# Kernel optimization log

Measured on AMD Instinct MI355X. Metric: run time of the kernel, lower is better.

## Reference

```python
import jax, jax.numpy as jnp
import numpy as np

EMBED = 768
HEADS = 12
HEAD_DIM = EMBED // HEADS
NUM_BUCKETS = 32
MAX_DISTANCE = 128


def _relative_buckets(tgt_len, src_len):
    ctx = jnp.arange(tgt_len)[:, None]
    mem = jnp.arange(src_len)[None, :]
    rel = mem - ctx                                  # [T, S]
    nb = NUM_BUCKETS // 2                            # 16
    buckets = (rel > 0).astype(jnp.int32) * nb
    rp = jnp.abs(rel)
    max_exact = nb // 2                              # 8
    is_small = rp < max_exact
    rp_safe = jnp.maximum(rp, 1).astype(jnp.float32)
    large = max_exact + (
        jnp.log(rp_safe / max_exact) / np.log(MAX_DISTANCE / max_exact) * (nb - max_exact)
    ).astype(jnp.int32)
    large = jnp.minimum(large, nb - 1)
    buckets = buckets + jnp.where(is_small, rp, large)
    return buckets                                   # [T, S] int32


def setup_inputs() -> dict:
    key = jax.random.key(0)
    ks = jax.random.split(key, 12)
    T, B, E = 2048, 2, EMBED
    def xavier(k, shape, gain=1.0):
        fan_in, fan_out = shape[0], shape[1]
        a = gain * np.sqrt(6.0 / (fan_in + fan_out))
        return jax.random.uniform(k, shape, jnp.float32, -a, a)
    g = 1.0 / np.sqrt(2.0)
    return {
        "query": jax.random.normal(ks[0], (T, B, E), jnp.float32),
        "key": jax.random.normal(ks[1], (T, B, E), jnp.float32),
        "value": jax.random.normal(ks[2], (T, B, E), jnp.float32),
        "key_padding_mask": jnp.zeros((B, T), dtype=bool),
        # weights stored [in, out] (transpose of torch Linear)
        "Wq": xavier(ks[3], (E, E), g), "bq": jnp.zeros((E,), jnp.float32),
        "Wk": xavier(ks[4], (E, E), g), "bk": jnp.zeros((E,), jnp.float32),
        "Wv": xavier(ks[5], (E, E), g), "bv": jnp.zeros((E,), jnp.float32),
        "Wo": xavier(ks[6], (E, E), 1.0), "bo": jnp.zeros((E,), jnp.float32),
        "rel_bias": jax.random.normal(ks[7], (NUM_BUCKETS, HEADS), jnp.float32)
        * np.sqrt(2.0 / (NUM_BUCKETS + HEADS)),
    }


def reference(query, key, value, key_padding_mask, Wq, bq, Wk, bk, Wv, bv, Wo, bo, rel_bias):
    T, B, E = query.shape
    S = key.shape[0]
    scaling = HEAD_DIM ** -0.5
    q = (query @ Wq + bq) * scaling
    k = key @ Wk + bk
    v = value @ Wv + bv
    # [T,B,E] -> [B,H,T,D]
    def split_heads(x, L):
        return x.reshape(L, B, HEADS, HEAD_DIM).transpose(1, 2, 0, 3)
    qh, kh, vh = split_heads(q, T), split_heads(k, S), split_heads(v, S)
    # T5 relative position bias: [H, T, S]
    buckets = _relative_buckets(T, S)
    position_bias = rel_bias[buckets].transpose(2, 0, 1)  # [H,T,S]
    scores = jnp.einsum("bhtd,bhsd->bhts", qh, kh) + position_bias[None]
    scores = jnp.where(key_padding_mask[:, None, None, :], -jnp.inf, scores)
    probs = jax.nn.softmax(scores, axis=-1)
    attn = jnp.einsum("bhts,bhsd->bhtd", probs, vh)
    attn = attn.transpose(2, 0, 1, 3).reshape(T, B, E)
    return attn @ Wo + bo
```

## Files before the change

### kernel.cpp

```cpp
#include <hip/hip_runtime.h>
#include <hip/hip_bf16.h>

typedef __bf16 bf16;
typedef __bf16 bf16x8 __attribute__((ext_vector_type(8)));
typedef float f32x4 __attribute__((ext_vector_type(4)));

#define EMB 768
#define NH 12
#define HD 64
#define SEQ 2048
#define NBATCH 2
#define NREL (2 * SEQ - 1)

__device__ __forceinline__ int swz(int bo) { return bo ^ ((bo >> 3) & 0x70); }
__device__ __forceinline__ int swz256(int bo) { return bo ^ ((bo >> 4) & 0x70); }
__device__ __forceinline__ int kpos(int s) {
  return (s & 0x23) | ((s & 0x04) << 2) | ((s & 0x18) >> 1);
}

typedef __attribute__((address_space(3))) unsigned int lds_u32;
typedef __attribute__((address_space(1))) unsigned int glb_u32;
__device__ __forceinline__ void gld16(const void* g, void* l) {
  __builtin_amdgcn_global_load_lds((const glb_u32*)g, (lds_u32*)l, 16, 0, 0);
}

__global__ void k_bias_table(const float* __restrict__ rel_bias,
                             float* __restrict__ bias_tab) {
  int i = blockIdx.x * 256 + threadIdx.x;
  if (i >= NREL) return;
  int rel = i - (SEQ - 1);
  int bkt = (rel > 0) ? 16 : 0;
  int rp = rel < 0 ? -rel : rel;
  if (rp < 8) {
    bkt += rp;
  } else {
    float lf = (logf((float)rp * 0.125f) / 2.7725887222397811f) * 8.0f;
    int large = 8 + (int)lf;
    bkt += (large < 15) ? large : 15;
  }
  for (int h = 0; h < NH; ++h)
    bias_tab[h * NREL + i] = rel_bias[bkt * NH + h];
}

__global__ void k_maskbits(const unsigned char* __restrict__ mask,
                           unsigned long long* __restrict__ mbits) {
  int wid = blockIdx.x * 4 + (threadIdx.x >> 6);
  int lane = threadIdx.x & 63;
  int b = wid >> 5, wd = wid & 31;
  unsigned long long m = __ballot(mask[b * SEQ + wd * 64 + lane] != 0);
  if (lane == 0) mbits[wid] = m;
}

__global__ __launch_bounds__(256) void k_cvt_x(
    const float* __restrict__ Xq, const float* __restrict__ Xk,
    const float* __restrict__ Xv, bf16* __restrict__ ximg) {
  const int z = blockIdx.z;
  const float* X = z == 0 ? Xq : z == 1 ? Xk : Xv;
  const int m0 = blockIdx.x * 128, k0 = blockIdx.y * 64;
  char* img = (char*)ximg + ((size_t)(z * 32 + blockIdx.x) * 12 + blockIdx.y) * 16384;
#pragma unroll
  for (int it = 0; it < 4; ++it) {
    int i = threadIdx.x + it * 256;
    int mr = i >> 3, kc8 = (i & 7) * 8;
    const float* xp = X + (size_t)(m0 + mr) * EMB + k0 + kc8;
    float4 f0 = *(const float4*)xp, f1 = *(const float4*)(xp + 4);
    bf16x8 hh;
    hh[0] = (bf16)f0.x; hh[1] = (bf16)f0.y; hh[2] = (bf16)f0.z; hh[3] = (bf16)f0.w;
    hh[4] = (bf16)f1.x; hh[5] = (bf16)f1.y; hh[6] = (bf16)f1.z; hh[7] = (bf16)f1.w;
    *(bf16x8*)(img + swz(mr * 128 + kc8 * 2)) = hh;
  }
}

__global__ __launch_bounds__(256) void k_cvt_w(
    const float* __restrict__ Wq, const float* __restrict__ Wk,
    const float* __restrict__ Wv, const float* __restrict__ Wo,
    bf16* __restrict__ wimg) {
  __shared__ __align__(16) bf16 T[64 * 128];
  const int z = blockIdx.z;
  const float* W = z == 0 ? Wq : z == 1 ? Wk : z == 2 ? Wv : Wo;
  const int nb = blockIdx.x, ks = blockIdx.y;
  const int n0 = nb * 128, k0 = ks * 64;
  const int tid = threadIdx.x;
  {
    int kk = tid >> 2, nn0 = (tid & 3) * 32;
    const float* wp = W + (size_t)(k0 + kk) * EMB + n0 + nn0;
#pragma unroll
    for (int jq = 0; jq < 4; ++jq) {
      float4 f0 = *(const float4*)(wp + jq * 8);
      float4 f1 = *(const float4*)(wp + jq * 8 + 4);
      bf16x8 hh;
      hh[0] = (bf16)f0.x; hh[1] = (bf16)f0.y; hh[2] = (bf16)f0.z; hh[3] = (bf16)f0.w;
      hh[4] = (bf16)f1.x; hh[5] = (bf16)f1.y; hh[6] = (bf16)f1.z; hh[7] = (bf16)f1.w;
      *(bf16x8*)((char*)T + swz256(kk * 256 + (nn0 + jq * 8) * 2)) = hh;
    }
  }
  __syncthreads();
  {
    int nr = tid >> 1, kh = tid & 1;
    char* img = (char*)wimg + ((size_t)(z * 6 + nb) * 12 + ks) * 16384;
#pragma unroll
    for (int jq = 0; jq < 4; ++jq) {
      union { bf16 e[8]; uint4 u; } pk;
#pragma unroll
      for (int q = 0; q < 8; ++q)
        pk.e[q] = *(const bf16*)((char*)T + swz256((kh * 32 + jq * 8 + q) * 256 + nr * 2));
      *(uint4*)(img + swz(nr * 128 + (kh * 32 + jq * 8) * 2)) = pk.u;
    }
  }
}

__global__ __launch_bounds__(256) void k_proj_qkv(
    const bf16* __restrict__ ximg, const bf16* __restrict__ wimg,
    const float* __restrict__ bq, const float* __restrict__ bk,
    const float* __restrict__ bv, bf16* __restrict__ oq,
    bf16* __restrict__ gk, bf16* __restrict__ gv) {
  __shared__ __align__(16) bf16 AB[2][2][8192];
  const int z = blockIdx.z;
  const float* bias = z == 0 ? bq : z == 1 ? bk : bv;
  const float scale = z == 0 ? 0.125f : 1.0f;
  const int mb = blockIdx.x, nb = blockIdx.y;
  const int m0 = mb * 128, n0 = nb * 128;
  const int tid = threadIdx.x, lane = tid & 63, w = tid >> 6;
  const int c = lane & 15, g = lane >> 4;
  const int mo = (w >> 1) * 64, no = (w & 1) * 64;
  const char* abase = (const char*)ximg + (size_t)(z * 32 + mb) * 12 * 16384;
  const char* bbase = (const char*)wimg + (size_t)(z * 6 + nb) * 12 * 16384;

#define PISSUE(KS, BUF) do {                                               \
    const char* a_ = abase + (size_t)(KS) * 16384;                         \
    const char* b_ = bbase + (size_t)(KS) * 16384;                         \
    _Pragma("unroll") for (int ch = 0; ch < 4; ++ch) {                     \
      int ck = w * 4 + ch;                                                 \
      gld16(a_ + ck * 1024 + lane * 16, (char*)AB[BUF][0] + ck * 1024);    \
      gld16(b_ + ck * 1024 + lane * 16, (char*)AB[BUF][1] + ck * 1024);    \
    }                                                                      \
  } while (0)

  PISSUE(0, 0);
  f32x4 acc[4][4] = {};
  asm volatile("s_waitcnt vmcnt(0)" ::: "memory");
  __syncthreads();
  for (int ks = 0; ks < 12; ++ks) {
    const int cur = ks & 1;
    if (ks < 11) PISSUE(ks + 1, cur ^ 1);
    const char* As = (const char*)AB[cur][0];
    const char* Bs = (const char*)AB[cur][1];
    __builtin_amdgcn_s_setprio(1);
#pragma unroll
    for (int kk = 0; kk < 2; ++kk) {
      bf16x8 av[4], bvf[4];
#pragma unroll
      for (int mf = 0; mf < 4; ++mf)
        av[mf] = *(const bf16x8*)(As + swz((mo + mf * 16 + c) * 128 + kk * 64 + g * 16));
#pragma unroll
      for (int nf = 0; nf < 4; ++nf)
        bvf[nf] = *(const bf16x8*)(Bs + swz((no + nf * 16 + c) * 128 + kk * 64 + g * 16));
#pragma unroll
      for (int mf = 0; mf < 4; ++mf)
#pragma unroll
        for (int nf = 0; nf < 4; ++nf)
          acc[mf][nf] = __builtin_amdgcn_mfma_f32_16x16x32_bf16(bvf[nf], av[mf], acc[mf][nf], 0, 0, 0);
    }
    __builtin_amdgcn_s_setprio(0);
    if (ks < 11) {
      asm volatile("s_waitcnt vmcnt(0)" ::: "memory");
      __syncthreads();
    }
  }
#pragma unroll
  for (int nf = 0; nf < 4; ++nf) {
    int n = n0 + no + nf * 16 + g * 4;
    float4 b4 = *(const float4*)&bias[n];
#pragma unroll
    for (int mf = 0; mf < 4; ++mf) {
      int m = m0 + mo + mf * 16 + c;
      float v0 = (acc[mf][nf][0] + b4.x) * scale;
      float v1 = (acc[mf][nf][1] + b4.y) * scale;
      float v2 = (acc[mf][nf][2] + b4.z) * scale;
      float v3 = (acc[mf][nf][3] + b4.w) * scale;
      if (z == 0) {
        union { bf16 e[4]; uint2 u; } pk;
        pk.e[0] = (bf16)v0; pk.e[1] = (bf16)v1; pk.e[2] = (bf16)v2; pk.e[3] = (bf16)v3;
        *(uint2*)(oq + (size_t)m * EMB + n) = pk.u;
      } else if (z == 1) {
        int t = m >> 1, bb = m & 1;
        int hh = n >> 6, d = n & 63;
        union { bf16 e[4]; uint2 u; } pk;
        pk.e[0] = (bf16)v0; pk.e[1] = (bf16)v1; pk.e[2] = (bf16)v2; pk.e[3] = (bf16)v3;
        char* base = (char*)gk + ((size_t)(bb * NH + hh) * 32 + (t >> 6)) * 8192;
        *(uint2*)(base + swz(kpos(t & 63) * 128 + (d & ~7) * 2) + (d & 4) * 2) = pk.u;
      } else {
        int s = m >> 1, bb = m & 1;
        int hh = n >> 6, d0 = n & 63;
        char* base = (char*)gv + ((size_t)(bb * NH + hh) * 32 + (s >> 6)) * 8192;
        int sc2 = (s & 63) * 2;
        *(bf16*)(base + (((d0 + 0) * 128 + sc2) ^ (((d0 + 0) & 7) << 4))) = (bf16)v0;
        *(bf16*)(base + (((d0 + 1) * 128 + sc2) ^ (((d0 + 1) & 7) << 4))) = (bf16)v1;
        *(bf16*)(base + (((d0 + 2) * 128 + sc2) ^ (((d0 + 2) & 7) << 4))) = (bf16)v2;
        *(bf16*)(base + (((d0 + 3) * 128 + sc2) ^ (((d0 + 3) & 7) << 4))) = (bf16)v3;
      }
    }
  }
#undef PISSUE
}

__global__ __launch_bounds__(256) void k_proj_out(
    const bf16* __restrict__ aimg, const bf16* __restrict__ wimg,
    const float* __restrict__ bias, float* __restrict__ out) {
  __shared__ __align__(16) bf16 AB[2][2][8192];
  const int mb = blockIdx.x, nb = blockIdx.y;
  const int m0 = mb * 128, n0 = nb * 128;
  const int tid = threadIdx.x, lane = tid & 63, w = tid >> 6;
  const int c = lane & 15, g = lane >> 4;
  const int mo = (w >> 1) * 64, no = (w & 1) * 64;
  const char* abase = (const char*)aimg + (size_t)mb * 12 * 16384;
  const char* bbase = (const char*)wimg + (size_t)(3 * 6 + nb) * 12 * 16384;

#define PISSUE(KS, BUF) do {                                               \
    const char* a_ = abase + (size_t)(KS) * 16384;                         \
    const char* b_ = bbase + (size_t)(KS) * 16384;                         \
    _Pragma("unroll") for (int ch = 0; ch < 4; ++ch) {                     \
      int ck = w * 4 + ch;                                                 \
      gld16(a_ + ck * 1024 + lane * 16, (char*)AB[BUF][0] + ck * 1024);    \
      gld16(b_ + ck * 1024 + lane * 16, (char*)AB[BUF][1] + ck * 1024);    \
    }                                                                      \
  } while (0)

  PISSUE(0, 0);
  f32x4 acc[4][4] = {};
  asm volatile("s_waitcnt vmcnt(0)" ::: "memory");
  __syncthreads();
  for (int ks = 0; ks < 12; ++ks) {
    const int cur = ks & 1;
    if (ks < 11) PISSUE(ks + 1, cur ^ 1);
    const char* As = (const char*)AB[cur][0];
    const char* Bs = (const char*)AB[cur][1];
    __builtin_amdgcn_s_setprio(1);
#pragma unroll
    for (int kk = 0; kk < 2; ++kk) {
      bf16x8 av[4], bvf[4];
#pragma unroll
      for (int mf = 0; mf < 4; ++mf)
        av[mf] = *(const bf16x8*)(As + swz((mo + mf * 16 + c) * 128 + kk * 64 + g * 16));
#pragma unroll
      for (int nf = 0; nf < 4; ++nf)
        bvf[nf] = *(const bf16x8*)(Bs + swz((no + nf * 16 + c) * 128 + kk * 64 + g * 16));
#pragma unroll
      for (int mf = 0; mf < 4; ++mf)
#pragma unroll
        for (int nf = 0; nf < 4; ++nf)
          acc[mf][nf] = __builtin_amdgcn_mfma_f32_16x16x32_bf16(bvf[nf], av[mf], acc[mf][nf], 0, 0, 0);
    }
    __builtin_amdgcn_s_setprio(0);
    if (ks < 11) {
      asm volatile("s_waitcnt vmcnt(0)" ::: "memory");
      __syncthreads();
    }
  }
#pragma unroll
  for (int nf = 0; nf < 4; ++nf) {
    int n = n0 + no + nf * 16 + g * 4;
    float4 b4 = *(const float4*)&bias[n];
#pragma unroll
    for (int mf = 0; mf < 4; ++mf) {
      int m = m0 + mo + mf * 16 + c;
      float4 v;
      v.x = acc[mf][nf][0] + b4.x;
      v.y = acc[mf][nf][1] + b4.y;
      v.z = acc[mf][nf][2] + b4.z;
      v.w = acc[mf][nf][3] + b4.w;
      *(float4*)(out + (size_t)m * EMB + n) = v;
    }
  }
#undef PISSUE
}

__global__ __launch_bounds__(256, 4) void k_attn(
    const bf16* __restrict__ qb, const bf16* __restrict__ gk,
    const bf16* __restrict__ gv, const unsigned long long* __restrict__ mbits,
    const float* __restrict__ bias_tab, bf16* __restrict__ aimg) {
  __shared__ __align__(16) bf16 KV[2][2][4096];
  __shared__ float Bslow[384];
  const int bh = blockIdx.x;
  const int b = bh / NH, h = bh % NH;
  const int t0 = blockIdx.y * 64;
  const int tid = threadIdx.x;
  const int lane = tid & 63, w = tid >> 6;
  const int c = lane & 15, g = lane >> 4;
  const float NEGINF = -__builtin_inff();
  const int tl = w * 16 + c;

  const char* kimg = (const char*)gk + (size_t)bh * 32 * 8192;
  const char* vimg = (const char*)gv + (size_t)bh * 32 * 8192;

#define ISSUE(IT, BUF) do {                                                  \
    const char* ks_ = kimg + (size_t)(IT) * 8192;                            \
    const char* vs_ = vimg + (size_t)(IT) * 8192;                            \
    _Pragma("unroll") for (int jj = 0; jj < 2; ++jj) {                       \
      int ch = w * 2 + jj;                                                   \
      gld16(ks_ + ch * 1024 + lane * 16, (char*)KV[BUF][0] + ch * 1024);     \
      gld16(vs_ + ch * 1024 + lane * 16, (char*)KV[BUF][1] + ch * 1024);     \
    }                                                                        \
  } while (0)

  ISSUE(0, 0);
  bf16x8 qf[2];
  {
    const bf16* qp = qb + (size_t)((t0 + tl) * NBATCH + b) * EMB + h * 64 + g * 8;
    qf[0] = *(const bf16x8*)qp;
    qf[1] = *(const bf16x8*)(qp + 32);
  }
  const float* btab = bias_tab + h * NREL + (SEQ - 1);
  for (int j = tid; j < 384; j += 256) Bslow[j] = btab[j - 192];
  const float cpos = btab[SEQ - 1];
  const float cneg = btab[-(SEQ - 1)];

  float m_p = -1e30f, l_p = 0.f;
  f32x4 o[4] = {};

  asm volatile("s_waitcnt vmcnt(0)" ::: "memory");
  __syncthreads();

  for (int it = 0; it < SEQ / 64; ++it) {
    const int cur = it & 1;
    if (it < SEQ / 64 - 1) ISSUE(it + 1, cur ^ 1);
    const unsigned long long mb = mbits[b * 32 + it];
    const char* Ks = (const char*)KV[cur][0];
    const char* Vs = (const char*)KV[cur][1];

    f32x4 sacc[4] = {};
    __builtin_amdgcn_s_setprio(1);
#pragma unroll
    for (int kk = 0; kk < 2; ++kk) {
#pragma unroll
      for (int nf = 0; nf < 4; ++nf) {
        bf16x8 kf = *(const bf16x8*)(Ks + swz((nf * 16 + c) * 128 + kk * 64 + g * 16));
        sacc[nf] = __builtin_amdgcn_mfma_f32_16x16x32_bf16(kf, qf[kk], sacc[nf], 0, 0, 0);
      }
    }
    __builtin_amdgcn_s_setprio(0);

    const int s0 = it * 64;
    const int d = s0 - t0;
    const bool slow = (d > -192) && (d < 192);
    const float cb = slow ? 0.f : (d >= 192 ? cpos : cneg);

    float rmax = NEGINF;
    if (slow) {
      const int bidx = d - tl + 192;
#pragma unroll
      for (int nf = 0; nf < 4; ++nf) {
        int sb = 32 * (nf >> 1) + g * 8 + (nf & 1) * 4;
#pragma unroll
        for (int r = 0; r < 4; ++r) sacc[nf][r] += Bslow[bidx + sb + r];
      }
    }
    if (mb) {
#pragma unroll
      for (int nf = 0; nf < 4; ++nf) {
        int sb = 32 * (nf >> 1) + g * 8 + (nf & 1) * 4;
#pragma unroll
        for (int r = 0; r < 4; ++r)
          if ((mb >> (sb + r)) & 1) sacc[nf][r] = NEGINF;
      }
    }
#pragma unroll
    for (int nf = 0; nf < 4; ++nf)
#pragma unroll
      for (int r = 0; r < 4; ++r) rmax = fmaxf(rmax, sacc[nf][r]);
    rmax = fmaxf(rmax, __shfl_xor(rmax, 16, 64));
    rmax = fmaxf(rmax, __shfl_xor(rmax, 32, 64));
    const float rm = rmax + cb;

    if (!__all(rm <= m_p + 8.0f)) {
      float m_new = fmaxf(m_p, rm);
      float scl = __expf(m_p - m_new);
      m_p = m_new;
      l_p *= scl;
#pragma unroll
      for (int r = 0; r < 4; ++r) {
        float so = __shfl(scl, g * 4 + r, 64);
#pragma unroll
        for (int nf2 = 0; nf2 < 4; ++nf2) o[nf2][r] *= so;
      }
    }
    const float msh = m_p - cb;
    float rsum = 0.f;
    bf16x8 pa[2];
#pragma unroll
    for (int kk = 0; kk < 2; ++kk)
#pragma unroll
      for (int j = 0; j < 8; ++j) {
        float e = __expf(sacc[2 * kk + (j >> 2)][j & 3] - msh);
        rsum += e;
        pa[kk][j] = (bf16)e;
      }
    rsum += __shfl_xor(rsum, 16, 64);
    rsum += __shfl_xor(rsum, 32, 64);
    l_p += rsum;

    __builtin_amdgcn_s_setprio(1);
#pragma unroll
    for (int kk = 0; kk < 2; ++kk) {
#pragma unroll
      for (int nf2 = 0; nf2 < 4; ++nf2) {
        bf16x8 vbf = *(const bf16x8*)(Vs + swz((nf2 * 16 + c) * 128 + kk * 64 + g * 16));
        o[nf2] = __builtin_amdgcn_mfma_f32_16x16x32_bf16(pa[kk], vbf, o[nf2], 0, 0, 0);
      }
    }
    __builtin_amdgcn_s_setprio(0);

    if (it < SEQ / 64 - 1) {
      asm volatile("s_waitcnt vmcnt(0)" ::: "memory");
      __syncthreads();
    }
  }
#pragma unroll
  for (int r = 0; r < 4; ++r) {
    float lo = __shfl(l_p, g * 4 + r, 64);
    float inv = 1.0f / lo;
    int t = t0 + w * 16 + g * 4 + r;
    int m = t * NBATCH + b;
    char* base = (char*)aimg + ((size_t)(m >> 7) * 12 + h) * 16384;
    int mr128 = (m & 127) * 128;
#pragma unroll
    for (int nf2 = 0; nf2 < 4; ++nf2) {
      int dd = nf2 * 16 + c;
      *(bf16*)(base + swz(mr128 + dd * 2)) = (bf16)(o[nf2][r] * inv);
    }
  }
#undef ISSUE
}

extern "C" void kernel_launch(void* const* d_in, const int* in_sizes, int n_in,
                              void* d_out, int out_size, void* d_ws, size_t ws_size,
                              hipStream_t stream) {
  const float* query = (const float*)d_in[0];
  const float* key_ = (const float*)d_in[1];
  const float* value = (const float*)d_in[2];
  const unsigned char* kpm = (const unsigned char*)d_in[3];
  const float* Wq = (const float*)d_in[4];
  const float* bq = (const float*)d_in[5];
  const float* Wk = (const float*)d_in[6];
  const float* bk = (const float*)d_in[7];
  const float* Wv = (const float*)d_in[8];
  const float* bv = (const float*)d_in[9];
  const float* Wo = (const float*)d_in[10];
  const float* bo = (const float*)d_in[11];
  const float* rel_bias = (const float*)d_in[12];
  float* out = (float*)d_out;

  char* ws = (char*)d_ws;
  const size_t SZb = (size_t)SEQ * NBATCH * EMB * sizeof(bf16);
  const size_t WIMG = (size_t)4 * 6 * 12 * 16384;
  bf16* qbb = (bf16*)(ws);
  bf16* gkb = (bf16*)(ws + SZb);
  bf16* gvb = (bf16*)(ws + 2 * SZb);
  bf16* wimg = (bf16*)(ws + 3 * SZb);
  float* bias_tab = (float*)(ws + 3 * SZb + WIMG);
  unsigned long long* mbits =
      (unsigned long long*)(ws + 3 * SZb + WIMG + 196608);
  bf16* ximg = (bf16*)(ws + 3 * SZb + WIMG + 196608 + 512);
  bf16* aimg = ximg;

  k_bias_table<<<16, 256, 0, stream>>>(rel_bias, bias_tab);
  k_maskbits<<<16, 256, 0, stream>>>(kpm, mbits);
  k_cvt_w<<<dim3(6, 12, 4), 256, 0, stream>>>(Wq, Wk, Wv, Wo, wimg);
  k_cvt_x<<<dim3(32, 12, 3), 256, 0, stream>>>(query, key_, value, ximg);
  k_proj_qkv<<<dim3(32, 6, 3), 256, 0, stream>>>(
      ximg, wimg, bq, bk, bv, qbb, gkb, gvb);
  k_attn<<<dim3(NBATCH * NH, SEQ / 64), 256, 0, stream>>>(
      qbb, gkb, gvb, mbits, bias_tab, aimg);
  k_proj_out<<<dim3(32, 6), 256, 0, stream>>>(aimg, wimg, bo, out);
}
```

Baseline: 110.2 us.

## Triple-buffer K/V tiles in attention and tree-reduce row max/sum

```diff
diff --git a/kernel.cpp b/kernel.cpp
--- a/kernel.cpp
+++ b/kernel.cpp
@@ -279,7 +279,7 @@
     const bf16* __restrict__ qb, const bf16* __restrict__ gk,
     const bf16* __restrict__ gv, const unsigned long long* __restrict__ mbits,
     const float* __restrict__ bias_tab, bf16* __restrict__ aimg) {
-  __shared__ __align__(16) bf16 KV[2][2][4096];
+  __shared__ __align__(16) bf16 KV[3][2][4096];
   __shared__ float Bslow[384];
   const int bh = blockIdx.x;
   const int b = bh / NH, h = bh % NH;
@@ -296,20 +296,22 @@
 #define ISSUE(IT, BUF) do {                                                  \
     const char* ks_ = kimg + (size_t)(IT) * 8192;                            \
     const char* vs_ = vimg + (size_t)(IT) * 8192;                            \
+    char* kd_ = (char*)KV + (BUF) * 16384;                                   \
     _Pragma("unroll") for (int jj = 0; jj < 2; ++jj) {                       \
       int ch = w * 2 + jj;                                                   \
-      gld16(ks_ + ch * 1024 + lane * 16, (char*)KV[BUF][0] + ch * 1024);     \
-      gld16(vs_ + ch * 1024 + lane * 16, (char*)KV[BUF][1] + ch * 1024);     \
+      gld16(ks_ + ch * 1024 + lane * 16, kd_ + ch * 1024);                   \
+      gld16(vs_ + ch * 1024 + lane * 16, kd_ + 8192 + ch * 1024);            \
     }                                                                        \
   } while (0)
 
-  ISSUE(0, 0);
   bf16x8 qf[2];
   {
     const bf16* qp = qb + (size_t)((t0 + tl) * NBATCH + b) * EMB + h * 64 + g * 8;
     qf[0] = *(const bf16x8*)qp;
     qf[1] = *(const bf16x8*)(qp + 32);
   }
+  ISSUE(0, 0);
+  ISSUE(1, 1);
   const float* btab = bias_tab + h * NREL + (SEQ - 1);
   for (int j = tid; j < 384; j += 256) Bslow[j] = btab[j - 192];
   const float cpos = btab[SEQ - 1];
@@ -318,15 +320,18 @@
   float m_p = -1e30f, l_p = 0.f;
   f32x4 o[4] = {};
 
-  asm volatile("s_waitcnt vmcnt(0)" ::: "memory");
-  __syncthreads();
-
-  for (int it = 0; it < SEQ / 64; ++it) {
-    const int cur = it & 1;
-    if (it < SEQ / 64 - 1) ISSUE(it + 1, cur ^ 1);
+  asm volatile("s_waitcnt vmcnt(4) lgkmcnt(0)" ::: "memory");
+  __builtin_amdgcn_s_barrier();
+
+  int cur = 0;
+  for (int it = 0; it < 32; ++it) {
+    const char* Ks = (const char*)KV + cur * 16384;
+    const char* Vs = Ks + 8192;
+    if (it < 30) {
+      int nb = cur >= 1 ? cur - 1 : 2;
+      ISSUE(it + 2, nb);
+    }
     const unsigned long long mb = mbits[b * 32 + it];
-    const char* Ks = (const char*)KV[cur][0];
-    const char* Vs = (const char*)KV[cur][1];
 
     f32x4 sacc[4] = {};
     __builtin_amdgcn_s_setprio(1);
@@ -345,7 +350,6 @@
     const bool slow = (d > -192) && (d < 192);
     const float cb = slow ? 0.f : (d >= 192 ? cpos : cneg);
 
-    float rmax = NEGINF;
     if (slow) {
       const int bidx = d - tl + 192;
 #pragma unroll
@@ -364,10 +368,11 @@
           if ((mb >> (sb + r)) & 1) sacc[nf][r] = NEGINF;
       }
     }
-#pragma unroll
-    for (int nf = 0; nf < 4; ++nf)
-#pragma unroll
-      for (int r = 0; r < 4; ++r) rmax = fmaxf(rmax, sacc[nf][r]);
+    f32x4 mx;
+#pragma unroll
+    for (int r = 0; r < 4; ++r)
+      mx[r] = fmaxf(fmaxf(sacc[0][r], sacc[1][r]), fmaxf(sacc[2][r], sacc[3][r]));
+    float rmax = fmaxf(fmaxf(mx[0], mx[1]), fmaxf(mx[2], mx[3]));
     rmax = fmaxf(rmax, __shfl_xor(rmax, 16, 64));
     rmax = fmaxf(rmax, __shfl_xor(rmax, 32, 64));
     const float rm = rmax + cb;
@@ -385,16 +390,17 @@
       }
     }
     const float msh = m_p - cb;
-    float rsum = 0.f;
+    f32x4 rs = {0.f, 0.f, 0.f, 0.f};
     bf16x8 pa[2];
 #pragma unroll
     for (int kk = 0; kk < 2; ++kk)
 #pragma unroll
       for (int j = 0; j < 8; ++j) {
         float e = __expf(sacc[2 * kk + (j >> 2)][j & 3] - msh);
-        rsum += e;
+        rs[j & 3] += e;
         pa[kk][j] = (bf16)e;
       }
+    float rsum = (rs[0] + rs[1]) + (rs[2] + rs[3]);
     rsum += __shfl_xor(rsum, 16, 64);
     rsum += __shfl_xor(rsum, 32, 64);
     l_p += rsum;
@@ -410,10 +416,14 @@
     }
     __builtin_amdgcn_s_setprio(0);
 
-    if (it < SEQ / 64 - 1) {
+    if (it < 30) {
+      asm volatile("s_waitcnt vmcnt(4)" ::: "memory");
+      __builtin_amdgcn_s_barrier();
+    } else if (it == 30) {
       asm volatile("s_waitcnt vmcnt(0)" ::: "memory");
-      __syncthreads();
-    }
+      __builtin_amdgcn_s_barrier();
+    }
+    cur = cur < 2 ? cur + 1 : 0;
   }
 #pragma unroll
   for (int r = 0; r < 4; ++r) {
```

Result: slower. 115.0 us (+4.3%).

## Split attention KV tile across wave pairs and switch softmax to exp2

Applied to the files above, without the earlier changes.

```diff
diff --git a/kernel.cpp b/kernel.cpp
--- a/kernel.cpp
+++ b/kernel.cpp
@@ -11,6 +11,7 @@
 #define SEQ 2048
 #define NBATCH 2
 #define NREL (2 * SEQ - 1)
+#define LOG2E 1.44269504088896f
 
 __device__ __forceinline__ int swz(int bo) { return bo ^ ((bo >> 3) & 0x70); }
 __device__ __forceinline__ int swz256(int bo) { return bo ^ ((bo >> 4) & 0x70); }
@@ -39,7 +40,7 @@
     bkt += (large < 15) ? large : 15;
   }
   for (int h = 0; h < NH; ++h)
-    bias_tab[h * NREL + i] = rel_bias[bkt * NH + h];
+    bias_tab[h * NREL + i] = rel_bias[bkt * NH + h] * LOG2E;
 }
 
 __global__ void k_maskbits(const unsigned char* __restrict__ mask,
@@ -117,7 +118,7 @@
   __shared__ __align__(16) bf16 AB[2][2][8192];
   const int z = blockIdx.z;
   const float* bias = z == 0 ? bq : z == 1 ? bk : bv;
-  const float scale = z == 0 ? 0.125f : 1.0f;
+  const float scale = z == 0 ? 0.125f * LOG2E : 1.0f;
   const int mb = blockIdx.x, nb = blockIdx.y;
   const int m0 = mb * 128, n0 = nb * 128;
   const int tid = threadIdx.x, lane = tid & 63, w = tid >> 6;
@@ -275,7 +276,7 @@
 #undef PISSUE
 }
 
-__global__ __launch_bounds__(256, 4) void k_attn(
+__global__ __launch_bounds__(256, 3) void k_attn(
     const bf16* __restrict__ qb, const bf16* __restrict__ gk,
     const bf16* __restrict__ gv, const unsigned long long* __restrict__ mbits,
     const float* __restrict__ bias_tab, bf16* __restrict__ aimg) {
@@ -287,8 +288,8 @@
   const int tid = threadIdx.x;
   const int lane = tid & 63, w = tid >> 6;
   const int c = lane & 15, g = lane >> 4;
+  const int tg = w >> 1, sh2 = w & 1;
   const float NEGINF = -__builtin_inff();
-  const int tl = w * 16 + c;
 
   const char* kimg = (const char*)gk + (size_t)bh * 32 * 8192;
   const char* vimg = (const char*)gv + (size_t)bh * 32 * 8192;
@@ -304,38 +305,40 @@
   } while (0)
 
   ISSUE(0, 0);
-  bf16x8 qf[2];
-  {
-    const bf16* qp = qb + (size_t)((t0 + tl) * NBATCH + b) * EMB + h * 64 + g * 8;
-    qf[0] = *(const bf16x8*)qp;
-    qf[1] = *(const bf16x8*)(qp + 32);
+  bf16x8 qf[2][2];
+#pragma unroll
+  for (int tf = 0; tf < 2; ++tf) {
+    const bf16* qp = qb + (size_t)((t0 + tg * 32 + tf * 16 + c) * NBATCH + b) * EMB + h * 64 + g * 8;
+    qf[tf][0] = *(const bf16x8*)qp;
+    qf[tf][1] = *(const bf16x8*)(qp + 32);
   }
   const float* btab = bias_tab + h * NREL + (SEQ - 1);
   for (int j = tid; j < 384; j += 256) Bslow[j] = btab[j - 192];
   const float cpos = btab[SEQ - 1];
   const float cneg = btab[-(SEQ - 1)];
 
-  float m_p = -1e30f, l_p = 0.f;
-  f32x4 o[4] = {};
+  float m_p[2] = {-1e30f, -1e30f}, l_p[2] = {0.f, 0.f};
+  f32x4 o[2][4] = {};
 
   asm volatile("s_waitcnt vmcnt(0)" ::: "memory");
   __syncthreads();
 
-  for (int it = 0; it < SEQ / 64; ++it) {
+  for (int it = 0; it < 32; ++it) {
     const int cur = it & 1;
-    if (it < SEQ / 64 - 1) ISSUE(it + 1, cur ^ 1);
+    if (it < 31) ISSUE(it + 1, cur ^ 1);
     const unsigned long long mb = mbits[b * 32 + it];
     const char* Ks = (const char*)KV[cur][0];
     const char* Vs = (const char*)KV[cur][1];
 
-    f32x4 sacc[4] = {};
+    f32x4 sacc[2][2] = {};
     __builtin_amdgcn_s_setprio(1);
 #pragma unroll
     for (int kk = 0; kk < 2; ++kk) {
 #pragma unroll
-      for (int nf = 0; nf < 4; ++nf) {
-        bf16x8 kf = *(const bf16x8*)(Ks + swz((nf * 16 + c) * 128 + kk * 64 + g * 16));
-        sacc[nf] = __builtin_amdgcn_mfma_f32_16x16x32_bf16(kf, qf[kk], sacc[nf], 0, 0, 0);
+      for (int sf = 0; sf < 2; ++sf) {
+        bf16x8 kf = *(const bf16x8*)(Ks + swz(((sh2 * 2 + sf) * 16 + c) * 128 + kk * 64 + g * 16));
+        sacc[0][sf] = __builtin_amdgcn_mfma_f32_16x16x32_bf16(kf, qf[0][kk], sacc[0][sf], 0, 0, 0);
+        sacc[1][sf] = __builtin_amdgcn_mfma_f32_16x16x32_bf16(kf, qf[1][kk], sacc[1][sf], 0, 0, 0);
       }
     }
     __builtin_amdgcn_s_setprio(0);
@@ -345,89 +348,139 @@
     const bool slow = (d > -192) && (d < 192);
     const float cb = slow ? 0.f : (d >= 192 ? cpos : cneg);
 
-    float rmax = NEGINF;
     if (slow) {
-      const int bidx = d - tl + 192;
-#pragma unroll
-      for (int nf = 0; nf < 4; ++nf) {
-        int sb = 32 * (nf >> 1) + g * 8 + (nf & 1) * 4;
-#pragma unroll
-        for (int r = 0; r < 4; ++r) sacc[nf][r] += Bslow[bidx + sb + r];
+#pragma unroll
+      for (int tf = 0; tf < 2; ++tf) {
+        const int bidx = d - (tg * 32 + tf * 16 + c) + 192 + 32 * sh2 + g * 8;
+#pragma unroll
+        for (int sf = 0; sf < 2; ++sf)
+#pragma unroll
+          for (int r = 0; r < 4; ++r) sacc[tf][sf][r] += Bslow[bidx + sf * 4 + r];
       }
     }
     if (mb) {
 #pragma unroll
-      for (int nf = 0; nf < 4; ++nf) {
-        int sb = 32 * (nf >> 1) + g * 8 + (nf & 1) * 4;
-#pragma unroll
-        for (int r = 0; r < 4; ++r)
-          if ((mb >> (sb + r)) & 1) sacc[nf][r] = NEGINF;
+      for (int tf = 0; tf < 2; ++tf)
+#pragma unroll
+        for (int sf = 0; sf < 2; ++sf) {
+          int sb = 32 * sh2 + g * 8 + sf * 4;
+#pragma unroll
+          for (int r = 0; r < 4; ++r)
+            if ((mb >> (sb + r)) & 1) sacc[tf][sf][r] = NEGINF;
+        }
+    }
+    float rm[2];
+#pragma unroll
+    for (int tf = 0; tf < 2; ++tf) {
+      f32x4 m4;
+#pragma unroll
+      for (int r = 0; r < 4; ++r) m4[r] = fmaxf(sacc[tf][0][r], sacc[tf][1][r]);
+      float rmax = fmaxf(fmaxf(m4[0], m4[1]), fmaxf(m4[2], m4[3]));
+      rmax = fmaxf(rmax, __shfl_xor(rmax, 16, 64));
+      rmax = fmaxf(rmax, __shfl_xor(rmax, 32, 64));
+      rm[tf] = rmax + cb;
+    }
+    bool okd = (rm[0] <= m_p[0] + 11.5f) && (rm[1] <= m_p[1] + 11.5f);
+    if (!__all(okd)) {
+#pragma unroll
+      for (int tf = 0; tf < 2; ++tf) {
+        float m_new = fmaxf(m_p[tf], rm[tf]);
+        float scl = exp2f(m_p[tf] - m_new);
+        m_p[tf] = m_new;
+        l_p[tf] *= scl;
+#pragma unroll
+        for (int r = 0; r < 4; ++r) {
+          float so = __shfl(scl, g * 4 + r, 64);
+#pragma unroll
+          for (int df = 0; df < 4; ++df) o[tf][df][r] *= so;
+        }
       }
     }
-#pragma unroll
-    for (int nf = 0; nf < 4; ++nf)
-#pragma unroll
-      for (int r = 0; r < 4; ++r) rmax = fmaxf(rmax, sacc[nf][r]);
-    rmax = fmaxf(rmax, __shfl_xor(rmax, 16, 64));
-    rmax = fmaxf(rmax, __shfl_xor(rmax, 32, 64));
-    const float rm = rmax + cb;
-
-    if (!__all(rm <= m_p + 8.0f)) {
-      float m_new = fmaxf(m_p, rm);
-      float scl = __expf(m_p - m_new);
-      m_p = m_new;
-      l_p *= scl;
-#pragma unroll
-      for (int r = 0; r < 4; ++r) {
-        float so = __shfl(scl, g * 4 + r, 64);
-#pragma unroll
-        for (int nf2 = 0; nf2 < 4; ++nf2) o[nf2][r] *= so;
+    bf16x8 pa[2];
+#pragma unroll
+    for (int tf = 0; tf < 2; ++tf) {
+      const float msh = m_p[tf] - cb;
+      f32x4 rs = {0.f, 0.f, 0.f, 0.f};
+#pragma unroll
+      for (int j = 0; j < 8; ++j) {
+        float e = exp2f(sacc[tf][j >> 2][j & 3] - msh);
+        rs[j & 3] += e;
+        pa[tf][j] = (bf16)e;
       }
-    }
-    const float msh = m_p - cb;
-    float rsum = 0.f;
-    bf16x8 pa[2];
-#pragma unroll
-    for (int kk = 0; kk < 2; ++kk)
-#pragma unroll
-      for (int j = 0; j < 8; ++j) {
-        float e = __expf(sacc[2 * kk + (j >> 2)][j & 3] - msh);
-        rsum += e;
-        pa[kk][j] = (bf16)e;
-      }
-    rsum += __shfl_xor(rsum, 16, 64);
-    rsum += __shfl_xor(rsum, 32, 64);
-    l_p += rsum;
-
+      float rsum = (rs[0] + rs[1]) + (rs[2] + rs[3]);
+      rsum += __shfl_xor(rsum, 16, 64);
+      rsum += __shfl_xor(rsum, 32, 64);
+      l_p[tf] += rsum;
+    }
     __builtin_amdgcn_s_setprio(1);
 #pragma unroll
-    for (int kk = 0; kk < 2; ++kk) {
-#pragma unroll
-      for (int nf2 = 0; nf2 < 4; ++nf2) {
-        bf16x8 vbf = *(const bf16x8*)(Vs + swz((nf2 * 16 + c) * 128 + kk * 64 + g * 16));
-        o[nf2] = __builtin_amdgcn_mfma_f32_16x16x32_bf16(pa[kk], vbf, o[nf2], 0, 0, 0);
-      }
+    for (int df = 0; df < 4; ++df) {
+      bf16x8 vbf = *(const bf16x8*)(Vs + swz((df * 16 + c) * 128 + sh2 * 64 + g * 16));
+      o[0][df] = __builtin_amdgcn_mfma_f32_16x16x32_bf16(pa[0], vbf, o[0][df], 0, 0, 0);
+      o[1][df] = __builtin_amdgcn_mfma_f32_16x16x32_bf16(pa[1], vbf, o[1][df], 0, 0, 0);
     }
     __builtin_amdgcn_s_setprio(0);
 
-    if (it < SEQ / 64 - 1) {
+    if (it < 31) {
       asm volatile("s_waitcnt vmcnt(0)" ::: "memory");
       __syncthreads();
     }
   }
-#pragma unroll
-  for (int r = 0; r < 4; ++r) {
-    float lo = __shfl(l_p, g * 4 + r, 64);
-    float inv = 1.0f / lo;
-    int t = t0 + w * 16 + g * 4 + r;
-    int m = t * NBATCH + b;
-    char* base = (char*)aimg + ((size_t)(m >> 7) * 12 + h) * 16384;
-    int mr128 = (m & 127) * 128;
-#pragma unroll
-    for (int nf2 = 0; nf2 < 4; ++nf2) {
-      int dd = nf2 * 16 + c;
-      *(bf16*)(base + swz(mr128 + dd * 2)) = (bf16)(o[nf2][r] * inv);
-    }
+  __syncthreads();
+  float* mlb = (float*)&KV[0][0][0];
+  float* ob  = mlb + 256;
+  if (g == 0) {
+#pragma unroll
+    for (int tf = 0; tf < 2; ++tf) {
+      int slot = ((tg * 2 + sh2) * 2 + tf) * 32;
+      mlb[slot + c] = m_p[tf];
+      mlb[slot + 16 + c] = l_p[tf];
+    }
+  }
+  __syncthreads();
+  float asf[2][4], lst[2][4];
+#pragma unroll
+  for (int tf = 0; tf < 2; ++tf)
+#pragma unroll
+    for (int r = 0; r < 4; ++r) {
+      int rr = g * 4 + r;
+      int s_own = ((tg * 2 + sh2) * 2 + tf) * 32;
+      int s_oth = ((tg * 2 + (sh2 ^ 1)) * 2 + tf) * 32;
+      float ms = mlb[s_own + rr], ls = mlb[s_own + 16 + rr];
+      float mo2 = mlb[s_oth + rr], lo2 = mlb[s_oth + 16 + rr];
+      float mst = fmaxf(ms, mo2);
+      float a = exp2f(ms - mst), b2 = exp2f(mo2 - mst);
+      asf[tf][r] = a;
+      lst[tf][r] = ls * a + lo2 * b2;
+    }
+  if (sh2 == 1) {
+#pragma unroll
+    for (int tf = 0; tf < 2; ++tf)
+#pragma unroll
+      for (int df = 0; df < 4; ++df)
+#pragma unroll
+        for (int r = 0; r < 4; ++r)
+          ob[((((tg * 2 + tf) * 4 + df) * 4 + r) * 4 + g) * 16 + c] = o[tf][df][r] * asf[tf][r];
+  }
+  __syncthreads();
+  if (sh2 == 0) {
+#pragma unroll
+    for (int tf = 0; tf < 2; ++tf)
+#pragma unroll
+      for (int r = 0; r < 4; ++r) {
+        float inv = 1.0f / lst[tf][r];
+        int t = t0 + tg * 32 + tf * 16 + g * 4 + r;
+        int m = t * NBATCH + b;
+        char* base = (char*)aimg + ((size_t)(m >> 7) * 12 + h) * 16384;
+        int mr128 = (m & 127) * 128;
+#pragma unroll
+        for (int df = 0; df < 4; ++df) {
+          float vsum = o[tf][df][r] * asf[tf][r] +
+                       ob[((((tg * 2 + tf) * 4 + df) * 4 + r) * 4 + g) * 16 + c];
+          int dd = df * 16 + c;
+          *(bf16*)(base + swz(mr128 + dd * 2)) = (bf16)(vsum * inv);
+        }
+      }
   }
 #undef ISSUE
 }
```

New measurement: 123.3 us. +11.8%, slower.

## Split attention KV range across two wave groups and use exp2 with MFMA row sums

Applied to the files above, without the earlier changes.

```diff
diff --git a/kernel.cpp b/kernel.cpp
--- a/kernel.cpp
+++ b/kernel.cpp
@@ -11,6 +11,7 @@
 #define SEQ 2048
 #define NBATCH 2
 #define NREL (2 * SEQ - 1)
+#define LOG2E 1.44269504088896f
 
 __device__ __forceinline__ int swz(int bo) { return bo ^ ((bo >> 3) & 0x70); }
 __device__ __forceinline__ int swz256(int bo) { return bo ^ ((bo >> 4) & 0x70); }
@@ -39,7 +40,7 @@
     bkt += (large < 15) ? large : 15;
   }
   for (int h = 0; h < NH; ++h)
-    bias_tab[h * NREL + i] = rel_bias[bkt * NH + h];
+    bias_tab[h * NREL + i] = rel_bias[bkt * NH + h] * LOG2E;
 }
 
 __global__ void k_maskbits(const unsigned char* __restrict__ mask,
@@ -117,7 +118,7 @@
   __shared__ __align__(16) bf16 AB[2][2][8192];
   const int z = blockIdx.z;
   const float* bias = z == 0 ? bq : z == 1 ? bk : bv;
-  const float scale = z == 0 ? 0.125f : 1.0f;
+  const float scale = z == 0 ? 0.125f * LOG2E : 1.0f;
   const int mb = blockIdx.x, nb = blockIdx.y;
   const int m0 = mb * 128, n0 = nb * 128;
   const int tid = threadIdx.x, lane = tid & 63, w = tid >> 6;
@@ -275,35 +276,37 @@
 #undef PISSUE
 }
 
-__global__ __launch_bounds__(256, 4) void k_attn(
+__global__ __launch_bounds__(512, 4) void k_attn(
     const bf16* __restrict__ qb, const bf16* __restrict__ gk,
     const bf16* __restrict__ gv, const unsigned long long* __restrict__ mbits,
     const float* __restrict__ bias_tab, bf16* __restrict__ aimg) {
-  __shared__ __align__(16) bf16 KV[2][2][4096];
+  __shared__ __align__(16) bf16 KV[2][2][2][4096];
   __shared__ float Bslow[384];
   const int bh = blockIdx.x;
   const int b = bh / NH, h = bh % NH;
   const int t0 = blockIdx.y * 64;
   const int tid = threadIdx.x;
   const int lane = tid & 63, w = tid >> 6;
+  const int sh = w >> 2, w4 = w & 3;
   const int c = lane & 15, g = lane >> 4;
   const float NEGINF = -__builtin_inff();
-  const int tl = w * 16 + c;
+  const int tl = w4 * 16 + c;
 
   const char* kimg = (const char*)gk + (size_t)bh * 32 * 8192;
   const char* vimg = (const char*)gv + (size_t)bh * 32 * 8192;
 
-#define ISSUE(IT, BUF) do {                                                  \
-    const char* ks_ = kimg + (size_t)(IT) * 8192;                            \
-    const char* vs_ = vimg + (size_t)(IT) * 8192;                            \
+#define ISSUE(ITA, BUF) do {                                                 \
+    const char* ks_ = kimg + (size_t)(ITA) * 8192;                           \
+    const char* vs_ = vimg + (size_t)(ITA) * 8192;                           \
+    char* kd_ = (char*)KV + ((sh * 2 + (BUF)) * 2) * 8192;                   \
     _Pragma("unroll") for (int jj = 0; jj < 2; ++jj) {                       \
-      int ch = w * 2 + jj;                                                   \
-      gld16(ks_ + ch * 1024 + lane * 16, (char*)KV[BUF][0] + ch * 1024);     \
-      gld16(vs_ + ch * 1024 + lane * 16, (char*)KV[BUF][1] + ch * 1024);     \
+      int ch = w4 * 2 + jj;                                                  \
+      gld16(ks_ + ch * 1024 + lane * 16, kd_ + ch * 1024);                   \
+      gld16(vs_ + ch * 1024 + lane * 16, kd_ + 8192 + ch * 1024);            \
     }                                                                        \
   } while (0)
 
-  ISSUE(0, 0);
+  ISSUE(sh * 16, 0);
   bf16x8 qf[2];
   {
     const bf16* qp = qb + (size_t)((t0 + tl) * NBATCH + b) * EMB + h * 64 + g * 8;
@@ -311,22 +314,28 @@
     qf[1] = *(const bf16x8*)(qp + 32);
   }
   const float* btab = bias_tab + h * NREL + (SEQ - 1);
-  for (int j = tid; j < 384; j += 256) Bslow[j] = btab[j - 192];
+  for (int j = tid; j < 384; j += 512) Bslow[j] = btab[j - 192];
   const float cpos = btab[SEQ - 1];
   const float cneg = btab[-(SEQ - 1)];
 
-  float m_p = -1e30f, l_p = 0.f;
+  bf16x8 ones8;
+#pragma unroll
+  for (int j = 0; j < 8; ++j) ones8[j] = (bf16)1.0f;
+
+  float m_p = -1e30f;
+  f32x4 lacc = {0.f, 0.f, 0.f, 0.f};
   f32x4 o[4] = {};
 
   asm volatile("s_waitcnt vmcnt(0)" ::: "memory");
   __syncthreads();
 
-  for (int it = 0; it < SEQ / 64; ++it) {
+  for (int it = 0; it < 16; ++it) {
+    const int ita = sh * 16 + it;
     const int cur = it & 1;
-    if (it < SEQ / 64 - 1) ISSUE(it + 1, cur ^ 1);
-    const unsigned long long mb = mbits[b * 32 + it];
-    const char* Ks = (const char*)KV[cur][0];
-    const char* Vs = (const char*)KV[cur][1];
+    if (it < 15) ISSUE(ita + 1, cur ^ 1);
+    const unsigned long long mb = mbits[b * 32 + ita];
+    const char* Ks = (const char*)KV + ((sh * 2 + cur) * 2) * 8192;
+    const char* Vs = Ks + 8192;
 
     f32x4 sacc[4] = {};
     __builtin_amdgcn_s_setprio(1);
@@ -340,12 +349,11 @@
     }
     __builtin_amdgcn_s_setprio(0);
 
-    const int s0 = it * 64;
+    const int s0 = ita * 64;
     const int d = s0 - t0;
     const bool slow = (d > -192) && (d < 192);
     const float cb = slow ? 0.f : (d >= 192 ? cpos : cneg);
 
-    float rmax = NEGINF;
     if (slow) {
       const int bidx = d - tl + 192;
 #pragma unroll
@@ -364,42 +372,38 @@
           if ((mb >> (sb + r)) & 1) sacc[nf][r] = NEGINF;
       }
     }
-#pragma unroll
-    for (int nf = 0; nf < 4; ++nf)
-#pragma unroll
-      for (int r = 0; r < 4; ++r) rmax = fmaxf(rmax, sacc[nf][r]);
+    f32x4 mx;
+#pragma unroll
+    for (int r = 0; r < 4; ++r)
+      mx[r] = fmaxf(fmaxf(sacc[0][r], sacc[1][r]), fmaxf(sacc[2][r], sacc[3][r]));
+    float rmax = fmaxf(fmaxf(mx[0], mx[1]), fmaxf(mx[2], mx[3]));
     rmax = fmaxf(rmax, __shfl_xor(rmax, 16, 64));
     rmax = fmaxf(rmax, __shfl_xor(rmax, 32, 64));
     const float rm = rmax + cb;
 
-    if (!__all(rm <= m_p + 8.0f)) {
+    if (!__all(rm <= m_p + 11.5f)) {
       float m_new = fmaxf(m_p, rm);
-      float scl = __expf(m_p - m_new);
+      float scl = exp2f(m_p - m_new);
       m_p = m_new;
-      l_p *= scl;
 #pragma unroll
       for (int r = 0; r < 4; ++r) {
         float so = __shfl(scl, g * 4 + r, 64);
+        lacc[r] *= so;
 #pragma unroll
         for (int nf2 = 0; nf2 < 4; ++nf2) o[nf2][r] *= so;
       }
     }
     const float msh = m_p - cb;
-    float rsum = 0.f;
     bf16x8 pa[2];
 #pragma unroll
     for (int kk = 0; kk < 2; ++kk)
 #pragma unroll
-      for (int j = 0; j < 8; ++j) {
-        float e = __expf(sacc[2 * kk + (j >> 2)][j & 3] - msh);
-        rsum += e;
-        pa[kk][j] = (bf16)e;
-      }
-    rsum += __shfl_xor(rsum, 16, 64);
-    rsum += __shfl_xor(rsum, 32, 64);
-    l_p += rsum;
+      for (int j = 0; j < 8; ++j)
+        pa[kk][j] = (bf16)exp2f(sacc[2 * kk + (j >> 2)][j & 3] - msh);
 
     __builtin_amdgcn_s_setprio(1);
+    lacc = __builtin_amdgcn_mfma_f32_16x16x32_bf16(pa[0], ones8, lacc, 0, 0, 0);
+    lacc = __builtin_amdgcn_mfma_f32_16x16x32_bf16(pa[1], ones8, lacc, 0, 0, 0);
 #pragma unroll
     for (int kk = 0; kk < 2; ++kk) {
 #pragma unroll
@@ -410,23 +414,56 @@
     }
     __builtin_amdgcn_s_setprio(0);
 
-    if (it < SEQ / 64 - 1) {
+    if (it < 15) {
       asm volatile("s_waitcnt vmcnt(0)" ::: "memory");
       __syncthreads();
     }
   }
+  __syncthreads();
+  float* mlb = (float*)KV;
+  float* ob = mlb + 256;
+  if (g == 0) mlb[(w4 * 2 + sh) * 32 + c] = m_p;
+  if (c == 0) {
+#pragma unroll
+    for (int r = 0; r < 4; ++r)
+      mlb[(w4 * 2 + sh) * 32 + 16 + g * 4 + r] = lacc[r];
+  }
+  __syncthreads();
+  float asf[4], lst[4];
 #pragma unroll
   for (int r = 0; r < 4; ++r) {
-    float lo = __shfl(l_p, g * 4 + r, 64);
-    float inv = 1.0f / lo;
-    int t = t0 + w * 16 + g * 4 + r;
-    int m = t * NBATCH + b;
-    char* base = (char*)aimg + ((size_t)(m >> 7) * 12 + h) * 16384;
-    int mr128 = (m & 127) * 128;
-#pragma unroll
-    for (int nf2 = 0; nf2 < 4; ++nf2) {
-      int dd = nf2 * 16 + c;
-      *(bf16*)(base + swz(mr128 + dd * 2)) = (bf16)(o[nf2][r] * inv);
+    int rr = g * 4 + r;
+    int s_own = (w4 * 2 + sh) * 32, s_oth = (w4 * 2 + (sh ^ 1)) * 32;
+    float ms = mlb[s_own + rr], ls = mlb[s_own + 16 + rr];
+    float mo2 = mlb[s_oth + rr], lo2 = mlb[s_oth + 16 + rr];
+    float M = fmaxf(ms, mo2);
+    float a = exp2f(ms - M), b2 = exp2f(mo2 - M);
+    asf[r] = a;
+    lst[r] = ls * a + lo2 * b2;
+  }
+  if (sh == 1) {
+#pragma unroll
+    for (int nf2 = 0; nf2 < 4; ++nf2)
+#pragma unroll
+      for (int r = 0; r < 4; ++r)
+        ob[(((w4 * 4 + nf2) * 4 + r) * 4 + g) * 16 + c] = o[nf2][r] * asf[r];
+  }
+  __syncthreads();
+  if (sh == 0) {
+#pragma unroll
+    for (int r = 0; r < 4; ++r) {
+      float inv = 1.0f / lst[r];
+      int t = t0 + w4 * 16 + g * 4 + r;
+      int m = t * NBATCH + b;
+      char* base = (char*)aimg + ((size_t)(m >> 7) * 12 + h) * 16384;
+      int mr128 = (m & 127) * 128;
+#pragma unroll
+      for (int nf2 = 0; nf2 < 4; ++nf2) {
+        float vsum = o[nf2][r] * asf[r] +
+                     ob[(((w4 * 4 + nf2) * 4 + r) * 4 + g) * 16 + c];
+        int dd = nf2 * 16 + c;
+        *(bf16*)(base + swz(mr128 + dd * 2)) = (bf16)(vsum * inv);
+      }
     }
   }
 #undef ISSUE
@@ -469,7 +506,7 @@
   k_cvt_x<<<dim3(32, 12, 3), 256, 0, stream>>>(query, key_, value, ximg);
   k_proj_qkv<<<dim3(32, 6, 3), 256, 0, stream>>>(
       ximg, wimg, bq, bk, bv, qbb, gkb, gvb);
-  k_attn<<<dim3(NBATCH * NH, SEQ / 64), 256, 0, stream>>>(
+  k_attn<<<dim3(NBATCH * NH, SEQ / 64), 512, 0, stream>>>(
       qbb, gkb, gvb, mbits, bias_tab, aimg);
   k_proj_out<<<dim3(32, 6), 256, 0, stream>>>(aimg, wimg, bo, out);
 }
```

Result: slower. 127.6 us (+15.8%).
